# Kernel tuning notes

Measured on AMD Instinct MI355X. Metric: run time of the kernel, lower is better.

Reference implementation:

```python
import jax, jax.numpy as jnp
import numpy as np

B, L, D, H, DFF = 16, 2048, 256, 8, 1024
CYCLES = 2
DEP = D // H
EPS = 1e-6


def _mha(q, k, v, Wq, Wk, Wv, Wo, bo):
    # q: [N, Lq, D], k/v: [N, Lk, D]  (mask is None in the source for both calls)
    N, Lq, _ = q.shape
    Lk = k.shape[1]
    qh = (q @ Wq).reshape(N, Lq, H, DEP)
    kh = (k @ Wk).reshape(N, Lk, H, DEP)
    vh = (v @ Wv).reshape(N, Lk, H, DEP)
    logits = jnp.einsum('nqhd,nkhd->nhqk', qh, kh) / jnp.sqrt(jnp.float32(DEP))
    w = jax.nn.softmax(logits, axis=-1)
    o = jnp.einsum('nhqk,nkhd->nqhd', w, vh).reshape(N, Lq, D)
    return o @ Wo + bo


def _layernorm(x, g, b):
    mu = jnp.mean(x, axis=-1, keepdims=True)
    var = jnp.mean(jnp.square(x - mu), axis=-1, keepdims=True)
    return g * (x - mu) * jax.lax.rsqrt(var + EPS) + b


def setup_inputs() -> dict:
    key = jax.random.key(0)
    ks = jax.random.split(key, 10)
    sc = 1.0 / np.sqrt(D)
    return {
        'e': jax.random.normal(ks[0], (B, L, D), dtype=jnp.float32),
        'Wq': jax.random.normal(ks[1], (D, D), dtype=jnp.float32) * sc,
        'Wk': jax.random.normal(ks[2], (D, D), dtype=jnp.float32) * sc,
        'Wv': jax.random.normal(ks[3], (D, D), dtype=jnp.float32) * sc,
        'Wo': jax.random.normal(ks[4], (D, D), dtype=jnp.float32) * sc,
        'bo': jnp.zeros((D,), dtype=jnp.float32),
        'W1': jax.random.normal(ks[5], (D, DFF), dtype=jnp.float32) * sc,
        'b1': jnp.zeros((DFF,), dtype=jnp.float32),
        'W2': jax.random.normal(ks[6], (DFF, D), dtype=jnp.float32) * (1.0 / np.sqrt(DFF)),
        'b2': jnp.zeros((D,), dtype=jnp.float32),
        'g1': jnp.ones((D,), dtype=jnp.float32),
        'be1': jnp.zeros((D,), dtype=jnp.float32),
        'g2': jnp.ones((D,), dtype=jnp.float32),
        'be2': jnp.zeros((D,), dtype=jnp.float32),
        'training': False,
    }


def reference(e, Wq, Wk, Wv, Wo, bo, W1, b1, W2, b2, g1, be1, g2, be2, training):
    # training=False -> dropouts are identity (eval mode)
    b, l, d = e.shape
    h = e
    s = jnp.mean(h, axis=1)  # relay node [b, d]
    for _ in range(CYCLES):
        h_last = jnp.roll(h, -1, axis=1)  # cycle_shift(h, False)
        h_next = jnp.roll(h, 1, axis=1)   # cycle_shift(h, True)
        s_m = jnp.broadcast_to(s[:, None, :], h.shape)
        # context [b, l, 5, d] -> [b*l, 5, d]
        c = jnp.stack([h_last, h, h_next, e, s_m], axis=-2).reshape(b * l, 5, d)
        hq = h.reshape(b * l, 1, d)
        h = jax.nn.relu(_mha(hq, c, c, Wq, Wk, Wv, Wo, bo)).reshape(b, l, d)
        # relay attention (the source reuses multi_att_satellite weights here)
        sq = s[:, None, :]               # [b, 1, d]
        mc = jnp.concatenate([sq, h], axis=1)  # [b, l+1, d]
        s = jax.nn.relu(_mha(sq, mc, mc, Wq, Wk, Wv, Wo, bo)).reshape(b, d)
    out1 = _layernorm(e + h, g1, be1)
    ffn = jax.nn.relu(out1 @ W1 + b1) @ W2 + b2
    out2 = _layernorm(out1 + ffn, g2, be2)
    return out2, s
```

## Files before the change

kernel.cpp:

```cpp
#include <hip/hip_runtime.h>

typedef unsigned short u16;
typedef unsigned int u32;
typedef __attribute__((ext_vector_type(8))) short bf16x8;
typedef __attribute__((ext_vector_type(4))) float f32x4;

#define LCONST __launch_bounds__(256)

__device__ __forceinline__ u16 f2bf(float f) {
  u32 u = __float_as_uint(f);
  u32 r = (u + 0x7FFFu + ((u >> 16) & 1u)) >> 16;
  return (u16)r;
}
__device__ __forceinline__ float bflo(u32 w) { return __uint_as_float(w << 16); }
__device__ __forceinline__ float bfhi(u32 w) { return __uint_as_float(w & 0xFFFF0000u); }
__device__ __forceinline__ float b2f(u16 v) { return __uint_as_float(((u32)v) << 16); }

__device__ __forceinline__ float dot8(uint4 u, const float* q) {
  return q[0]*bflo(u.x) + q[1]*bfhi(u.x) + q[2]*bflo(u.y) + q[3]*bfhi(u.y)
       + q[4]*bflo(u.z) + q[5]*bfhi(u.z) + q[6]*bflo(u.w) + q[7]*bfhi(u.w);
}
__device__ __forceinline__ void fma8(uint4 u, float wt, float* a) {
  a[0] = fmaf(wt, bflo(u.x), a[0]); a[1] = fmaf(wt, bfhi(u.x), a[1]);
  a[2] = fmaf(wt, bflo(u.y), a[2]); a[3] = fmaf(wt, bfhi(u.y), a[3]);
  a[4] = fmaf(wt, bflo(u.z), a[4]); a[5] = fmaf(wt, bfhi(u.z), a[5]);
  a[6] = fmaf(wt, bflo(u.w), a[6]); a[7] = fmaf(wt, bfhi(u.w), a[7]);
}

__device__ __forceinline__ void gload16(const u16* g, u16* l) {
  __builtin_amdgcn_global_load_lds(
      (const __attribute__((address_space(1))) unsigned int*)g,
      (__attribute__((address_space(3))) unsigned int*)l, 16, 0, 0);
}

__global__ LCONST void prep_kernel(const float* __restrict__ e,
                                   const float* __restrict__ Wq, const float* __restrict__ Wk,
                                   const float* __restrict__ Wv, const float* __restrict__ Wo,
                                   const float* __restrict__ W1, const float* __restrict__ W2,
                                   u16* __restrict__ Wqkv_t, u16* __restrict__ Wo_t,
                                   u16* __restrict__ W1_t, u16* __restrict__ W2_t,
                                   float* __restrict__ part, u16* __restrict__ ebf) {
  int blk = blockIdx.x;
  int tid = threadIdx.x;
  if (blk < 3072) {
    int idx = blk * 256 + tid;
    if (idx < 196608) {
      int sub = idx >> 16, r = idx & 65535;
      int n = r >> 8, k = r & 255;
      const float* src = (sub == 0) ? Wq : ((sub == 1) ? Wk : Wv);
      Wqkv_t[idx] = f2bf(src[(size_t)k * 256 + n]);
    } else if (idx < 262144) {
      int r = idx - 196608;
      int n = r >> 8, k = r & 255;
      Wo_t[r] = f2bf(Wo[(size_t)k * 256 + n]);
    } else if (idx < 524288) {
      int r = idx - 262144;
      int n = r >> 8, k = r & 255;
      W1_t[r] = f2bf(W1[(size_t)k * 1024 + n]);
    } else {
      int r = idx - 524288;
      int n = r >> 10, k = r & 1023;
      W2_t[r] = f2bf(W2[(size_t)k * 256 + n]);
    }
  } else {
    int mb = blk - 3072;
    int b = mb >> 5, c = mb & 31;
    size_t base = ((size_t)b * 2048 + (size_t)c * 64) * 256 + tid;
    float s = 0.f;
    #pragma unroll 8
    for (int i = 0; i < 64; i++) {
      float v = e[base + (size_t)i * 256];
      s += v;
      ebf[base + (size_t)i * 256] = f2bf(v);
    }
    part[(size_t)mb * 256 + tid] = s;
  }
}

template <int BM, int BN, int EPI>
__device__ __forceinline__ void gemm_core(
    int bid, int nwg, u16* As, u16* Bs,
    const u16* __restrict__ A, const u16* __restrict__ Bt,
    const float* __restrict__ bias,
    u16* __restrict__ C0, u16* __restrict__ C1, u16* __restrict__ C2,
    const u16* __restrict__ resbf,
    const float* __restrict__ g, const float* __restrict__ be,
    float* __restrict__ Fout, int N, int K) {
  constexpr int WR = BM / 2;
  constexpr int MR = WR / 16;
  constexpr int ACH_PW = (BM / 8) / 8;
  constexpr int BCH_PW = 4;

  const int tid = threadIdx.x, lane = tid & 63, wid = tid >> 6;
  const int wm = wid >> 2, wn = wid & 3;

  const int ncol = N / BN;
  const int swz = (bid & 7) * (nwg >> 3) + (bid >> 3);
  const int mb = swz / ncol, nb = swz - mb * ncol;
  const int m0 = mb * BM, n0 = nb * BN;

  const int lrow8 = lane >> 3;
  const int cg = (lane & 7) ^ lrow8;

  f32x4 acc[MR][4] = {};
  for (int kt = 0; kt < K; kt += 64) {
    #pragma unroll
    for (int it = 0; it < ACH_PW; it++) {
      int ca = wid * ACH_PW + it;
      int row = ca * 8 + lrow8;
      gload16(A + (size_t)(m0 + row) * K + kt + cg * 8, As + ca * 512);
    }
    #pragma unroll
    for (int it = 0; it < BCH_PW; it++) {
      int cb = wid * BCH_PW + it;
      int row = cb * 8 + lrow8;
      gload16(Bt + (size_t)(n0 + row) * K + kt + cg * 8, Bs + cb * 512);
    }
    __syncthreads();
    const int lr = lane & 15, hi = lane >> 4;
    #pragma unroll
    for (int kk = 0; kk < 2; kk++) {
      const int slot = (kk * 4 + hi) ^ (lr & 7);
      bf16x8 af[MR], bfr[4];
      #pragma unroll
      for (int m = 0; m < MR; m++)
        af[m] = *(const bf16x8*)&As[(wm * WR + m * 16 + lr) * 64 + slot * 8];
      #pragma unroll
      for (int n = 0; n < 4; n++)
        bfr[n] = *(const bf16x8*)&Bs[(wn * 64 + n * 16 + lr) * 64 + slot * 8];
      #pragma unroll
      for (int m = 0; m < MR; m++)
        #pragma unroll
        for (int n = 0; n < 4; n++)
          acc[m][n] = __builtin_amdgcn_mfma_f32_16x16x32_bf16(af[m], bfr[n], acc[m][n], 0, 0, 0);
    }
    __syncthreads();
  }

  const int lr = lane & 15, hi = lane >> 4;
  if constexpr (EPI == 0) {
    const int bsel = n0 >> 8;
    u16* C = (bsel == 0) ? C0 : ((bsel == 1) ? C1 : C2);
    #pragma unroll
    for (int m = 0; m < MR; m++)
      #pragma unroll
      for (int n = 0; n < 4; n++)
        #pragma unroll
        for (int r = 0; r < 4; r++) {
          int row = m0 + wm * WR + m * 16 + hi * 4 + r;
          int col = wn * 64 + n * 16 + lr;
          C[(size_t)row * 256 + col] = f2bf(acc[m][n][r]);
        }
  } else if constexpr (EPI == 1) {
    #pragma unroll
    for (int m = 0; m < MR; m++)
      #pragma unroll
      for (int n = 0; n < 4; n++)
        #pragma unroll
        for (int r = 0; r < 4; r++) {
          int row = m0 + wm * WR + m * 16 + hi * 4 + r;
          int col = n0 + wn * 64 + n * 16 + lr;
          float v = fmaxf(acc[m][n][r] + bias[col], 0.f);
          C0[(size_t)row * N + col] = f2bf(v);
        }
  } else {
    __shared__ float rs_[BM], rq_[BM];
    if (tid < BM) { rs_[tid] = 0.f; rq_[tid] = 0.f; }
    __syncthreads();
    #pragma unroll
    for (int m = 0; m < MR; m++)
      #pragma unroll
      for (int n = 0; n < 4; n++)
        #pragma unroll
        for (int r = 0; r < 4; r++) {
          int rl = wm * WR + m * 16 + hi * 4 + r;
          int col = wn * 64 + n * 16 + lr;
          size_t gi = (size_t)(m0 + rl) * 256 + col;
          acc[m][n][r] = acc[m][n][r] + bias[col] + b2f(resbf[gi]);
        }
    #pragma unroll
    for (int m = 0; m < MR; m++)
      #pragma unroll
      for (int r = 0; r < 4; r++) {
        float s = 0.f, q = 0.f;
        #pragma unroll
        for (int n = 0; n < 4; n++) { float x = acc[m][n][r]; s += x; q += x * x; }
        #pragma unroll
        for (int off = 1; off < 16; off <<= 1) {
          s += __shfl_xor(s, off);
          q += __shfl_xor(q, off);
        }
        if (lr == 0) {
          int rl = wm * WR + m * 16 + hi * 4 + r;
          atomicAdd(&rs_[rl], s);
          atomicAdd(&rq_[rl], q);
        }
      }
    __syncthreads();
    #pragma unroll
    for (int m = 0; m < MR; m++)
      #pragma unroll
      for (int n = 0; n < 4; n++)
        #pragma unroll
        for (int r = 0; r < 4; r++) {
          int rl = wm * WR + m * 16 + hi * 4 + r;
          int col = wn * 64 + n * 16 + lr;
          size_t gi = (size_t)(m0 + rl) * 256 + col;
          float mu = rs_[rl] * (1.f / 256.f);
          float var = rq_[rl] * (1.f / 256.f) - mu * mu;
          float rstd = rsqrtf(fmaxf(var, 0.f) + 1e-6f);
          Fout[gi] = g[col] * (acc[m][n][r] - mu) * rstd + be[col];
        }
  }
}

template <int BM, int BN, int EPI>
__global__ __launch_bounds__(512, 4)
void gemm3_kernel(const u16* __restrict__ A, const u16* __restrict__ Bt,
                  const float* __restrict__ bias,
                  u16* __restrict__ C0, u16* __restrict__ C1, u16* __restrict__ C2,
                  const u16* __restrict__ resbf,
                  const float* __restrict__ g, const float* __restrict__ be,
                  float* __restrict__ Fout,
                  int M, int N, int K) {
  __shared__ __align__(16) u16 As[BM * 64];
  __shared__ __align__(16) u16 Bs[BN * 64];
  gemm_core<BM, BN, EPI>(blockIdx.x, gridDim.x, As, Bs, A, Bt, bias,
                         C0, C1, C2, resbf, g, be, Fout, N, K);
  (void)M;
}

__global__ LCONST void mha2a_kernel(const float* __restrict__ sqp, const float* __restrict__ skp,
                                    const float* __restrict__ svp, const u16* __restrict__ pk,
                                    const u16* __restrict__ pv, float* __restrict__ partial) {
  __shared__ float rmax[4], rsm[4], racc[4][32];
  const int blk = blockIdx.x;
  const int bh = blk >> 2, c = blk & 3;
  const int b = bh >> 3, h = bh & 7;
  const int tid = threadIdx.x;
  const int lane = tid & 63, wid = tid >> 6;
  const int off = h * 32;
  const float sc = 0.17677669529663687f;

  float qf[32];
  {
    const float* q = sqp + b * 256 + off;
    #pragma unroll
    for (int j = 0; j < 32; j++) qf[j] = q[j];
  }
  const int k0 = c * 512 + tid;
  const int k1 = k0 + 256;
  const u16* kp0 = pk + ((size_t)b * 2048 + k0) * 256 + off;
  const u16* kp1 = pk + ((size_t)b * 2048 + k1) * 256 + off;
  float d0 = 0.f, d1 = 0.f;
  #pragma unroll
  for (int cc = 0; cc < 4; cc++) {
    d0 += dot8(*(const uint4*)(kp0 + cc * 8), qf + cc * 8);
    d1 += dot8(*(const uint4*)(kp1 + cc * 8), qf + cc * 8);
  }
  d0 *= sc; d1 *= sc;
  float ds = -1e30f;
  if (c == 0 && tid == 0) {
    float dv = 0.f;
    const float* k = skp + b * 256 + off;
    #pragma unroll
    for (int j = 0; j < 32; j++) dv = fmaf(qf[j], k[j], dv);
    ds = dv * sc;
  }
  float lmax = fmaxf(fmaxf(d0, d1), ds);
  #pragma unroll
  for (int o = 32; o; o >>= 1) lmax = fmaxf(lmax, __shfl_down(lmax, o));
  if (lane == 0) rmax[wid] = lmax;
  __syncthreads();
  const float M = fmaxf(fmaxf(rmax[0], rmax[1]), fmaxf(rmax[2], rmax[3]));

  float w0 = __expf(d0 - M), w1 = __expf(d1 - M);
  float lsum = w0 + w1;
  float a[32];
  #pragma unroll
  for (int j = 0; j < 32; j++) a[j] = 0.f;
  const u16* vp0 = pv + ((size_t)b * 2048 + k0) * 256 + off;
  const u16* vp1 = pv + ((size_t)b * 2048 + k1) * 256 + off;
  #pragma unroll
  for (int cc = 0; cc < 4; cc++) {
    fma8(*(const uint4*)(vp0 + cc * 8), w0, a + cc * 8);
    fma8(*(const uint4*)(vp1 + cc * 8), w1, a + cc * 8);
  }
  if (c == 0 && tid == 0) {
    float ws = __expf(ds - M);
    lsum += ws;
    const float* v = svp + b * 256 + off;
    #pragma unroll
    for (int j = 0; j < 32; j++) a[j] = fmaf(ws, v[j], a[j]);
  }
  #pragma unroll
  for (int o = 32; o; o >>= 1) lsum += __shfl_down(lsum, o);
  if (lane == 0) rsm[wid] = lsum;
  #pragma unroll
  for (int j = 0; j < 32; j++) {
    float v = a[j];
    #pragma unroll
    for (int o = 32; o; o >>= 1) v += __shfl_down(v, o);
    if (lane == 0) racc[wid][j] = v;
  }
  __syncthreads();
  float* P = partial + (size_t)blk * 36;
  if (tid < 32) {
    P[2 + tid] = racc[0][tid] + racc[1][tid] + racc[2][tid] + racc[3][tid];
    if (tid == 0) {
      P[0] = M;
      P[1] = rsm[0] + rsm[1] + rsm[2] + rsm[3];
    }
  }
}

template <int EPI>
__global__ __launch_bounds__(512, 4)
void attnwo_kernel(const u16* __restrict__ hq, const u16* __restrict__ pk,
                   const u16* __restrict__ pv, const u16* __restrict__ ek,
                   const u16* __restrict__ ev, const float* __restrict__ skp,
                   const float* __restrict__ svp,
                   const u16* __restrict__ Wo_t, const float* __restrict__ bo,
                   u16* __restrict__ C0, u16* __restrict__ C1,
                   const u16* __restrict__ resbf,
                   const float* __restrict__ g, const float* __restrict__ be) {
  __shared__ __align__(16) u16 As[64 * 256];
  __shared__ __align__(16) u16 Bs[256 * 64];
  const int tid = threadIdx.x, lane = tid & 63, wid = tid >> 6;
  const int wm = wid >> 2, wn = wid & 3;
  const int nwg = gridDim.x, bid = blockIdx.x;
  const int swz = (bid & 7) * (nwg >> 3) + (bid >> 3);
  const int m0 = swz * 64;
  const int lrow8 = lane >> 3;
  const int cg = (lane & 7) ^ lrow8;

  #pragma unroll
  for (int it = 0; it < 4; it++) {
    int cb = wid * 4 + it;
    int row = cb * 8 + lrow8;
    gload16(Wo_t + (size_t)row * 256 + 0 * 64 + cg * 8, (u16*)Bs + cb * 512);
  }

  {
    const int r = tid >> 3, h = tid & 7;
    const size_t token = (size_t)(m0 + r);
    const int b = (int)(token >> 11);
    const int i = (int)(token & 2047);
    const size_t tb = (size_t)b << 11;
    const size_t ip = tb + ((i + 1) & 2047);
    const size_t im = tb + ((i + 2047) & 2047);
    const int off = h * 32;

    float qf[32];
    {
      const u16* q = hq + token * 256 + off;
      #pragma unroll
      for (int c = 0; c < 4; c++) {
        uint4 u = *(const uint4*)(q + c * 8);
        qf[c*8+0] = bflo(u.x); qf[c*8+1] = bfhi(u.x);
        qf[c*8+2] = bflo(u.y); qf[c*8+3] = bfhi(u.y);
        qf[c*8+4] = bflo(u.z); qf[c*8+5] = bfhi(u.z);
        qf[c*8+6] = bflo(u.w); qf[c*8+7] = bfhi(u.w);
      }
    }
    const u16* kr0 = pk + ip * 256 + off;
    const u16* kr1 = pk + token * 256 + off;
    const u16* kr2 = pk + im * 256 + off;
    const u16* kr3 = ek + token * 256 + off;
    float lg[5];
    {
      float d0 = 0, d1 = 0, d2 = 0, d3 = 0;
      #pragma unroll
      for (int cc = 0; cc < 4; cc++) {
        d0 += dot8(*(const uint4*)(kr0 + cc * 8), qf + cc * 8);
        d1 += dot8(*(const uint4*)(kr1 + cc * 8), qf + cc * 8);
        d2 += dot8(*(const uint4*)(kr2 + cc * 8), qf + cc * 8);
        d3 += dot8(*(const uint4*)(kr3 + cc * 8), qf + cc * 8);
      }
      lg[0] = d0; lg[1] = d1; lg[2] = d2; lg[3] = d3;
      float d4 = 0;
      const float* s = skp + b * 256 + off;
      #pragma unroll
      for (int j = 0; j < 32; j++) d4 = fmaf(qf[j], s[j], d4);
      lg[4] = d4;
    }
    const float sc = 0.17677669529663687f;
    float mx = lg[0];
    #pragma unroll
    for (int c = 1; c < 5; c++) mx = fmaxf(mx, lg[c]);
    float w[5], den = 0.f;
    #pragma unroll
    for (int c = 0; c < 5; c++) { w[c] = __expf((lg[c] - mx) * sc); den += w[c]; }

    float a[32];
    #pragma unroll
    for (int j = 0; j < 32; j++) a[j] = 0.f;
    const u16* vr0 = pv + ip * 256 + off;
    const u16* vr1 = pv + token * 256 + off;
    const u16* vr2 = pv + im * 256 + off;
    const u16* vr3 = ev + token * 256 + off;
    #pragma unroll
    for (int cc = 0; cc < 4; cc++) {
      fma8(*(const uint4*)(vr0 + cc * 8), w[0], a + cc * 8);
      fma8(*(const uint4*)(vr1 + cc * 8), w[1], a + cc * 8);
      fma8(*(const uint4*)(vr2 + cc * 8), w[2], a + cc * 8);
      fma8(*(const uint4*)(vr3 + cc * 8), w[3], a + cc * 8);
    }
    {
      const float* s = svp + b * 256 + off;
      #pragma unroll
      for (int j = 0; j < 32; j++) a[j] = fmaf(w[4], s[j], a[j]);
    }
    const float inv = 1.f / den;
    #pragma unroll
    for (int c = 0; c < 4; c++) {
      uint4 u;
      u.x = (u32)f2bf(a[c*8+0] * inv) | ((u32)f2bf(a[c*8+1] * inv) << 16);
      u.y = (u32)f2bf(a[c*8+2] * inv) | ((u32)f2bf(a[c*8+3] * inv) << 16);
      u.z = (u32)f2bf(a[c*8+4] * inv) | ((u32)f2bf(a[c*8+5] * inv) << 16);
      u.w = (u32)f2bf(a[c*8+6] * inv) | ((u32)f2bf(a[c*8+7] * inv) << 16);
      int s = h * 4 + c;
      int sp = (s & 24) | ((s & 7) ^ (r & 7));
      *(uint4*)&As[r * 256 + sp * 8] = u;
    }
  }
  __syncthreads();

  const int lr = lane & 15, hi = lane >> 4;
  f32x4 acc[2][4] = {};
  for (int kt = 0; kt < 4; kt++) {
    #pragma unroll
    for (int kk = 0; kk < 2; kk++) {
      bf16x8 af[2], bfr[4];
      #pragma unroll
      for (int m = 0; m < 2; m++) {
        int row = wm * 32 + m * 16 + lr;
        int sp = kt * 8 + ((kk * 4 + hi) ^ (row & 7));
        af[m] = *(const bf16x8*)&As[row * 256 + sp * 8];
      }
      const int slotB = (kk * 4 + hi) ^ (lr & 7);
      #pragma unroll
      for (int n = 0; n < 4; n++)
        bfr[n] = *(const bf16x8*)&Bs[(wn * 64 + n * 16 + lr) * 64 + slotB * 8];
      #pragma unroll
      for (int m = 0; m < 2; m++)
        #pragma unroll
        for (int n = 0; n < 4; n++)
          acc[m][n] = __builtin_amdgcn_mfma_f32_16x16x32_bf16(af[m], bfr[n], acc[m][n], 0, 0, 0);
    }
    __syncthreads();
    if (kt < 3) {
      #pragma unroll
      for (int it = 0; it < 4; it++) {
        int cb = wid * 4 + it;
        int row = cb * 8 + lrow8;
        gload16(Wo_t + (size_t)row * 256 + (kt + 1) * 64 + cg * 8, (u16*)Bs + cb * 512);
      }
      __syncthreads();
    }
  }

  if constexpr (EPI == 1) {
    #pragma unroll
    for (int m = 0; m < 2; m++)
      #pragma unroll
      for (int n = 0; n < 4; n++)
        #pragma unroll
        for (int r = 0; r < 4; r++) {
          int row = m0 + wm * 32 + m * 16 + hi * 4 + r;
          int col = wn * 64 + n * 16 + lr;
          float v = fmaxf(acc[m][n][r] + bo[col], 0.f);
          C0[(size_t)row * 256 + col] = f2bf(v);
        }
  } else {
    __shared__ float rsum[64], rsq[64];
    if (tid < 64) { rsum[tid] = 0.f; rsq[tid] = 0.f; }
    __syncthreads();
    #pragma unroll
    for (int m = 0; m < 2; m++)
      #pragma unroll
      for (int n = 0; n < 4; n++)
        #pragma unroll
        for (int r = 0; r < 4; r++) {
          int rl = wm * 32 + m * 16 + hi * 4 + r;
          int col = wn * 64 + n * 16 + lr;
          size_t gi = (size_t)(m0 + rl) * 256 + col;
          float v = fmaxf(acc[m][n][r] + bo[col], 0.f);
          C0[gi] = f2bf(v);
          acc[m][n][r] = b2f(resbf[gi]) + v;
        }
    #pragma unroll
    for (int m = 0; m < 2; m++)
      #pragma unroll
      for (int r = 0; r < 4; r++) {
        float s = 0.f, q = 0.f;
        #pragma unroll
        for (int n = 0; n < 4; n++) { float x = acc[m][n][r]; s += x; q += x * x; }
        #pragma unroll
        for (int off = 1; off < 16; off <<= 1) {
          s += __shfl_xor(s, off);
          q += __shfl_xor(q, off);
        }
        if (lr == 0) {
          int rl = wm * 32 + m * 16 + hi * 4 + r;
          atomicAdd(&rsum[rl], s);
          atomicAdd(&rsq[rl], q);
        }
      }
    __syncthreads();
    #pragma unroll
    for (int m = 0; m < 2; m++)
      #pragma unroll
      for (int n = 0; n < 4; n++)
        #pragma unroll
        for (int r = 0; r < 4; r++) {
          int rl = wm * 32 + m * 16 + hi * 4 + r;
          int col = wn * 64 + n * 16 + lr;
          size_t gi = (size_t)(m0 + rl) * 256 + col;
          float mu = rsum[rl] * (1.f / 256.f);
          float var = rsq[rl] * (1.f / 256.f) - mu * mu;
          float rstd = rsqrtf(fmaxf(var, 0.f) + 1e-6f);
          C1[gi] = f2bf(g[col] * (acc[m][n][r] - mu) * rstd + be[col]);
        }
  }
}

template <bool MEAN>
__global__ LCONST void proj_kernel(const float* __restrict__ X, const float* __restrict__ part,
                                   const float* __restrict__ Wq, const float* __restrict__ Wk,
                                   const float* __restrict__ Wv, float* __restrict__ Yq,
                                   float* __restrict__ Yk, float* __restrict__ Yv) {
  __shared__ float xs[256];
  __shared__ float red[256];
  const int b = blockIdx.x;
  const int wsel = blockIdx.y >> 2, n0 = (blockIdx.y & 3) * 64;
  const int tid = threadIdx.x;
  if constexpr (MEAN) {
    float s = 0.f;
    #pragma unroll
    for (int c = 0; c < 32; c++) s += part[((size_t)b * 32 + c) * 256 + tid];
    xs[tid] = s * (1.f / 2048.f);
  } else {
    xs[tid] = X[b * 256 + tid];
  }
  __syncthreads();
  const float* W = (wsel == 0) ? Wq : ((wsel == 1) ? Wk : Wv);
  float* Y = (wsel == 0) ? Yq : ((wsel == 1) ? Yk : Yv);
  const int c = tid & 63, g = tid >> 6;
  float p = 0.f;
  #pragma unroll 8
  for (int j = g * 64; j < g * 64 + 64; j++)
    p = fmaf(xs[j], W[(size_t)j * 256 + n0 + c], p);
  red[tid] = p;
  __syncthreads();
  if (g == 0)
    Y[b * 256 + n0 + c] = red[c] + red[64 + c] + red[128 + c] + red[192 + c];
}

__global__ __launch_bounds__(512, 4)
void qkvproj_kernel(const u16* __restrict__ ebf, const u16* __restrict__ Wqkv_t,
                    u16* __restrict__ hq, u16* __restrict__ ek, u16* __restrict__ ev,
                    const float* __restrict__ part,
                    const float* __restrict__ Wq, const float* __restrict__ Wk,
                    const float* __restrict__ Wv, float* __restrict__ Yq,
                    float* __restrict__ Yk, float* __restrict__ Yv) {
  extern __shared__ __align__(16) char smem[];
  const int bid = blockIdx.x, tid = threadIdx.x;
  if (bid < 768) {
    u16* As = (u16*)smem;
    u16* Bs = As + 128 * 64;
    gemm_core<128, 256, 0>(bid, 768, As, Bs, ebf, Wqkv_t, nullptr,
                           hq, ek, ev, nullptr, nullptr, nullptr, nullptr, 768, 256);
  } else {
    float* xs = (float*)smem;
    float* red = xs + 256;
    const int vb = bid - 768;
    const int b = vb & 15, y = vb >> 4;
    const int wsel = y >> 2, n0 = (y & 3) * 64;
    if (tid < 256) {
      float s = 0.f;
      #pragma unroll
      for (int c = 0; c < 32; c++) s += part[((size_t)b * 32 + c) * 256 + tid];
      xs[tid] = s * (1.f / 2048.f);
    }
    __syncthreads();
    const float* W = (wsel == 0) ? Wq : ((wsel == 1) ? Wk : Wv);
    float* Y = (wsel == 0) ? Yq : ((wsel == 1) ? Yk : Yv);
    const int c = tid & 63, g = tid >> 6;
    float p = 0.f;
    #pragma unroll 8
    for (int j = g * 32; j < g * 32 + 32; j++)
      p = fmaf(xs[j], W[(size_t)j * 256 + n0 + c], p);
    red[tid] = p;
    __syncthreads();
    if (g == 0) {
      float v = 0.f;
      #pragma unroll
      for (int k = 0; k < 8; k++) v += red[k * 64 + c];
      Y[b * 256 + n0 + c] = v;
    }
  }
}

__global__ __launch_bounds__(512, 4)
void kvffn_kernel(const u16* __restrict__ out1, const u16* __restrict__ W1_t,
                  const float* __restrict__ b1, u16* __restrict__ ffn1,
                  const u16* __restrict__ hbuf, const u16* __restrict__ Wkv_t,
                  u16* __restrict__ pk, u16* __restrict__ pv) {
  extern __shared__ __align__(16) char smem[];
  u16* As = (u16*)smem;
  u16* Bs = As + 128 * 64;
  const int bid = blockIdx.x;
  if (bid < 1024) {
    gemm_core<128, 256, 1>(bid, 1024, As, Bs, out1, W1_t, b1,
                           ffn1, nullptr, nullptr, nullptr, nullptr, nullptr, nullptr, 1024, 256);
  } else {
    gemm_core<128, 256, 0>(bid - 1024, 512, As, Bs, hbuf, Wkv_t, nullptr,
                           pk, pv, nullptr, nullptr, nullptr, nullptr, nullptr, 512, 256);
  }
}

__global__ LCONST void mha2c_kernel(const float* __restrict__ partial,
                                    const float* __restrict__ Wo, const float* __restrict__ bo,
                                    float* __restrict__ Y) {
  __shared__ float xs[256];
  __shared__ float red[256];
  const int b = blockIdx.x;
  const int n0 = blockIdx.y * 64;
  const int tid = threadIdx.x;
  {
    int hh = tid >> 5, d = tid & 31;
    const float* P = partial + (size_t)(b * 8 + hh) * 144;
    float M = fmaxf(fmaxf(P[0], P[36]), fmaxf(P[72], P[108]));
    float l = 0.f, o = 0.f;
    #pragma unroll
    for (int c = 0; c < 4; c++) {
      float f = __expf(P[c * 36] - M);
      l += f * P[c * 36 + 1];
      o += f * P[c * 36 + 2 + d];
    }
    xs[tid] = o / l;
  }
  __syncthreads();
  const int c = tid & 63, g = tid >> 6;
  float p = 0.f;
  #pragma unroll 8
  for (int j = g * 64; j < g * 64 + 64; j++)
    p = fmaf(xs[j], Wo[(size_t)j * 256 + n0 + c], p);
  red[tid] = p;
  __syncthreads();
  if (g == 0) {
    float v = red[c] + red[64 + c] + red[128 + c] + red[192 + c];
    Y[b * 256 + n0 + c] = fmaxf(v + bo[n0 + c], 0.f);
  }
}

extern "C" void kernel_launch(void* const* d_in, const int* in_sizes, int n_in,
                              void* d_out, int out_size, void* d_ws, size_t ws_size,
                              hipStream_t stream) {
  const float* e   = (const float*)d_in[0];
  const float* Wq  = (const float*)d_in[1];
  const float* Wk  = (const float*)d_in[2];
  const float* Wv  = (const float*)d_in[3];
  const float* Wo  = (const float*)d_in[4];
  const float* bo  = (const float*)d_in[5];
  const float* W1  = (const float*)d_in[6];
  const float* b1  = (const float*)d_in[7];
  const float* W2  = (const float*)d_in[8];
  const float* b2  = (const float*)d_in[9];
  const float* g1  = (const float*)d_in[10];
  const float* be1 = (const float*)d_in[11];
  const float* g2  = (const float*)d_in[12];
  const float* be2 = (const float*)d_in[13];

  char* wsb = (char*)d_ws;
  size_t off = 0;
  auto alc = [&](size_t n) { void* p = wsb + off; off += (n + 255) & ~(size_t)255; return p; };
  u16* Wqkv_t = (u16*)alc(768 * 256 * 2);
  u16* Wo_t   = (u16*)alc(65536 * 2);
  u16* W1_t   = (u16*)alc(262144 * 2);
  u16* W2_t   = (u16*)alc(262144 * 2);
  float* sB    = (float*)alc(4096 * 4);
  float* sqp   = (float*)alc(4096 * 4);
  float* skp   = (float*)alc(4096 * 4);
  float* svp   = (float*)alc(4096 * 4);
  float* partM = (float*)alc(512 * 36 * 4);
  float* part  = (float*)alc(524288);
  const size_t SZ = 16777216;
  u16* hq   = (u16*)alc(SZ);
  u16* ek   = (u16*)alc(SZ);
  u16* ev   = (u16*)alc(SZ);
  u16* ebf  = (u16*)alc(SZ);
  u16* pk   = (u16*)alc(SZ);
  u16* pv   = (u16*)alc(SZ);
  u16* hbuf = (u16*)alc(SZ);
  u16* out1 = (u16*)alc(SZ);
  u16* ffn1 = hq;

  const int M = 32768;
  float* outp  = (float*)d_out;
  float* s_out = outp + 8388608;

  prep_kernel<<<3584, 256, 0, stream>>>(e, Wq, Wk, Wv, Wo, W1, W2,
      Wqkv_t, Wo_t, W1_t, W2_t, part, ebf);

  qkvproj_kernel<<<960, 512, 49152, stream>>>(ebf, Wqkv_t, hq, ek, ev,
      part, Wq, Wk, Wv, sqp, skp, svp);
  attnwo_kernel<1><<<512, 512, 0, stream>>>(hq, ek, ev, ek, ev, skp, svp,
      Wo_t, bo, hbuf, nullptr, nullptr, nullptr, nullptr);
  gemm3_kernel<128, 256, 0><<<768, 512, 0, stream>>>(hbuf, Wqkv_t, nullptr, hq, pk, pv,
      nullptr, nullptr, nullptr, nullptr, M, 768, 256);
  mha2a_kernel<<<512, 256, 0, stream>>>(sqp, skp, svp, pk, pv, partM);
  mha2c_kernel<<<dim3(16, 4), 256, 0, stream>>>(partM, Wo, bo, sB);
  proj_kernel<false><<<dim3(16, 12), 256, 0, stream>>>(sB, nullptr, Wq, Wk, Wv, sqp, skp, svp);

  attnwo_kernel<2><<<512, 512, 0, stream>>>(hq, pk, pv, ek, ev, skp, svp,
      Wo_t, bo, hbuf, out1, ebf, g1, be1);
  kvffn_kernel<<<1536, 512, 49152, stream>>>(out1, W1_t, b1, ffn1,
      hbuf, Wqkv_t + 65536, pk, pv);
  mha2a_kernel<<<512, 256, 0, stream>>>(sqp, skp, svp, pk, pv, partM);
  mha2c_kernel<<<dim3(16, 4), 256, 0, stream>>>(partM, Wo, bo, s_out);
  gemm3_kernel<64, 256, 4><<<512, 512, 0, stream>>>(ffn1, W2_t, b2, nullptr, nullptr, nullptr,
      out1, g2, be2, outp, M, 256, 1024);
  (void)in_sizes; (void)n_in; (void)out_size; (void)ws_size;
}
```

Measured before the change: 260.3 us.

## Stream attention output through a smaller A tile to cut shared memory

```diff
diff --git a/kernel.cpp b/kernel.cpp
--- a/kernel.cpp
+++ b/kernel.cpp
@@ -315,7 +315,7 @@
 }
 
 template <int EPI>
-__global__ __launch_bounds__(512, 4)
+__global__ __launch_bounds__(512, 6)
 void attnwo_kernel(const u16* __restrict__ hq, const u16* __restrict__ pk,
                    const u16* __restrict__ pv, const u16* __restrict__ ek,
                    const u16* __restrict__ ev, const float* __restrict__ skp,
@@ -324,7 +324,7 @@
                    u16* __restrict__ C0, u16* __restrict__ C1,
                    const u16* __restrict__ resbf,
                    const float* __restrict__ g, const float* __restrict__ be) {
-  __shared__ __align__(16) u16 As[64 * 256];
+  __shared__ __align__(16) u16 As[64 * 64];
   __shared__ __align__(16) u16 Bs[256 * 64];
   const int tid = threadIdx.x, lane = tid & 63, wid = tid >> 6;
   const int wm = wid >> 2, wn = wid & 3;
@@ -333,6 +333,7 @@
   const int m0 = swz * 64;
   const int lrow8 = lane >> 3;
   const int cg = (lane & 7) ^ lrow8;
+  const int arow = tid >> 3, ah = tid & 7;
 
   #pragma unroll
   for (int it = 0; it < 4; it++) {
@@ -341,15 +342,15 @@
     gload16(Wo_t + (size_t)row * 256 + 0 * 64 + cg * 8, (u16*)Bs + cb * 512);
   }
 
+  u32 ov[16];
   {
-    const int r = tid >> 3, h = tid & 7;
-    const size_t token = (size_t)(m0 + r);
+    const size_t token = (size_t)(m0 + arow);
     const int b = (int)(token >> 11);
     const int i = (int)(token & 2047);
     const size_t tb = (size_t)b << 11;
     const size_t ip = tb + ((i + 1) & 2047);
     const size_t im = tb + ((i + 2047) & 2047);
-    const int off = h * 32;
+    const int off = ah * 32;
 
     float qf[32];
     {
@@ -413,15 +414,17 @@
     }
     const float inv = 1.f / den;
     #pragma unroll
+    for (int j = 0; j < 16; j++)
+      ov[j] = (u32)f2bf(a[2*j] * inv) | ((u32)f2bf(a[2*j+1] * inv) << 16);
+  }
+
+  if ((ah >> 1) == 0) {
+    const int base = (ah & 1) * 4;
+    #pragma unroll
     for (int c = 0; c < 4; c++) {
-      uint4 u;
-      u.x = (u32)f2bf(a[c*8+0] * inv) | ((u32)f2bf(a[c*8+1] * inv) << 16);
-      u.y = (u32)f2bf(a[c*8+2] * inv) | ((u32)f2bf(a[c*8+3] * inv) << 16);
-      u.z = (u32)f2bf(a[c*8+4] * inv) | ((u32)f2bf(a[c*8+5] * inv) << 16);
-      u.w = (u32)f2bf(a[c*8+6] * inv) | ((u32)f2bf(a[c*8+7] * inv) << 16);
-      int s = h * 4 + c;
-      int sp = (s & 24) | ((s & 7) ^ (r & 7));
-      *(uint4*)&As[r * 256 + sp * 8] = u;
+      int sp = (base + c) ^ (arow & 7);
+      uint4 u = make_uint4(ov[c*4], ov[c*4+1], ov[c*4+2], ov[c*4+3]);
+      *(uint4*)&As[arow * 64 + sp * 8] = u;
     }
   }
   __syncthreads();
@@ -435,8 +438,8 @@
       #pragma unroll
       for (int m = 0; m < 2; m++) {
         int row = wm * 32 + m * 16 + lr;
-        int sp = kt * 8 + ((kk * 4 + hi) ^ (row & 7));
-        af[m] = *(const bf16x8*)&As[row * 256 + sp * 8];
+        int sp = (kk * 4 + hi) ^ (row & 7);
+        af[m] = *(const bf16x8*)&As[row * 64 + sp * 8];
       }
       const int slotB = (kk * 4 + hi) ^ (lr & 7);
       #pragma unroll
@@ -455,6 +458,15 @@
         int cb = wid * 4 + it;
         int row = cb * 8 + lrow8;
         gload16(Wo_t + (size_t)row * 256 + (kt + 1) * 64 + cg * 8, (u16*)Bs + cb * 512);
+      }
+      if ((ah >> 1) == kt + 1) {
+        const int base = (ah & 1) * 4;
+        #pragma unroll
+        for (int c = 0; c < 4; c++) {
+          int sp = (base + c) ^ (arow & 7);
+          uint4 u = make_uint4(ov[c*4], ov[c*4+1], ov[c*4+2], ov[c*4+3]);
+          *(uint4*)&As[arow * 64 + sp * 8] = u;
+        }
       }
       __syncthreads();
     }
```

Result: slower. 346.6 us (+33.1%).
